# Performance work log

Measured on AMD Instinct MI355X. Metric: run time of the kernel, lower is better.

## Reference

```python
import jax, jax.numpy as jnp
import numpy as np

P = 16          # patch_size
IMG = 224       # image_size
NP = IMG // P   # 14 patches per side
TOTAL = NP * NP # 196
D = P * P * 3   # 768 features per patch


def setup_inputs() -> dict:
    key = jax.random.key(0)
    k1, k2, k3 = jax.random.split(key, 3)
    B = 256
    x = jax.random.normal(k1, (B, 3, IMG, IMG), dtype=jnp.float32)
    # Stacked per-patch Linear(768, 1) weights/biases (196 unshared extractors).
    weight = jax.random.normal(k2, (TOTAL, D), dtype=jnp.float32) * (1.0 / np.sqrt(D))
    bias = jax.random.normal(k3, (TOTAL,), dtype=jnp.float32) * 0.01
    return {"x": x, "weight": weight, "bias": bias}


def _extract_patches(x):
    # Faithful replication of torch: unfold(2,P,P).unfold(3,P,P) ->
    # [B,C,nH,nW,P,P]; permute(0,4,5,1,2,3) -> [B,P,P,C,nH,nW];
    # contiguous().view(B, 196, C, P, P)  (note: this view scrambles axes,
    # as in the original module; we replicate the exact reinterpretation).
    B, C, H, W = x.shape
    nH, nW = H // P, W // P
    p = x.reshape(B, C, nH, P, nW, P).transpose(0, 1, 2, 4, 3, 5)  # [B,C,nH,nW,P,P]
    p = p.transpose(0, 4, 5, 1, 2, 3)                               # [B,P,P,C,nH,nW]
    return p.reshape(B, TOTAL, D)                                   # flatten per 'patch'


def reference(x, weight, bias):
    patches = _extract_patches(x)                   # [B, 196, 768]
    # 196 unshared Linear(768,1) projections as one batched dot-product.
    scores = jnp.einsum('bpd,pd->bp', patches, weight) + bias  # [B, 196]
    return scores
```

## Files before the change

kernel.cpp:

```cpp
#include <hip/hip_runtime.h>


#define NPATCH 196
#define NF4IMG 37632
#define BSTR   197

__global__ __launch_bounds__(256) void prep_kernel(
    const float* __restrict__ weight,
    float* __restrict__ wlay)
{
    const int f = blockIdx.x * 256 + threadIdx.x;
    const int j    = f & 15;
    const int i    = (f >> 4) & 15;
    const int rest = f >> 8;
    const int w  = rest % 14;
    const int ch = rest / 14;
    const int h  = ch % 14;
    const int c  = ch / 14;
    wlay[f] = weight[i * 9408 + j * 588 + c * 196 + h * 14 + w];
}

__global__ __launch_bounds__(896) void run_kernel(
    const float* __restrict__ x,
    const float* __restrict__ wlay,
    const float* __restrict__ bias,
    float* __restrict__ out)
{
    __shared__ float bins[14 * BSTR];
    const int tid  = threadIdx.x;
    const int b    = blockIdx.x;
    const int wv   = tid >> 6;
    const int lane = tid & 63;
    const int i    = lane >> 2;
    const int j4   = lane & 3;

    for (int k = tid; k < 14 * BSTR; k += 896) bins[k] = 0.0f;
    __syncthreads();

    const int h = wv;
    float* mybins = bins + wv * BSTR;

    for (int c = 0; c < 3; ++c) {
        const int tile = c * 14 + h;
        const float4* __restrict__ x4 = (const float4*)x + (size_t)b * NF4IMG
                                        + c * 12544 + (16 * h + i) * 56 + j4;
        const float4* __restrict__ w4 = (const float4*)wlay + tile * 896 + i * 4 + j4;

        int p0[4], ws_[4];
        #pragma unroll
        for (int dj = 0; dj < 4; ++dj) {
            const int jj = 4 * j4 + dj;
            const int t0 = i * 9408 + jj * 588 + c * 196 + h * 14;
            p0[dj]  = t0 / 768;
            ws_[dj] = 768 * (p0[dj] + 1) - t0;
        }

        float accA[4] = {0.f, 0.f, 0.f, 0.f};
        float accB[4] = {0.f, 0.f, 0.f, 0.f};
        #pragma unroll
        for (int w = 0; w < 14; ++w) {
            const float4 xv  = x4[4 * w];
            const float4 wv_ = w4[64 * w];
            const float xs[4]  = {xv.x, xv.y, xv.z, xv.w};
            const float wsv[4] = {wv_.x, wv_.y, wv_.z, wv_.w};
            #pragma unroll
            for (int dj = 0; dj < 4; ++dj) {
                const float v   = xs[dj] * wsv[dj];
                const float sel = (w < ws_[dj]) ? 1.0f : 0.0f;
                accA[dj] = fmaf(v, sel, accA[dj]);
                accB[dj] = fmaf(v, 1.0f - sel, accB[dj]);
            }
        }

        #pragma unroll
        for (int dj = 0; dj < 4; ++dj) {
            unsafeAtomicAdd(&mybins[p0[dj]], accA[dj]);
            if (ws_[dj] < 14)
                unsafeAtomicAdd(&mybins[p0[dj] + 1], accB[dj]);
        }
    }
    __syncthreads();

    for (int p = tid; p < NPATCH; p += 896) {
        float s = 0.0f;
        #pragma unroll
        for (int k = 0; k < 14; ++k) s += bins[k * BSTR + p];
        out[b * NPATCH + p] = s + bias[p];
    }
}

extern "C" void kernel_launch(void* const* d_in, const int* in_sizes, int n_in,
                              void* d_out, int out_size, void* d_ws, size_t ws_size,
                              hipStream_t stream) {
    const float* x      = (const float*)d_in[0];
    const float* weight = (const float*)d_in[1];
    const float* bias   = (const float*)d_in[2];
    float* out          = (float*)d_out;
    float* wlay         = (float*)d_ws;

    prep_kernel<<<588, 256, 0, stream>>>(weight, wlay);
    run_kernel<<<256, 896, 0, stream>>>(x, wlay, bias, out);
}
```

Before: 37.78 us.

## Split each image across two blocks with atomic output, bias init in prep kernel

The main kernel now launches two 448-thread blocks per image, each covering half of the 14 patch rows. The halves combine their partial sums with global atomic adds into the output. The prep kernel pre-fills the output with bias and rewrites the weight permutation as coalesced float4 reads with scattered writes. The aim is more, smaller blocks for better occupancy and latency hiding, at the cost of global atomics and a dependence on the prep kernel initializing the output.

```diff
diff --git a/kernel.cpp b/kernel.cpp
--- a/kernel.cpp
+++ b/kernel.cpp
@@ -7,39 +7,61 @@
 
 __global__ __launch_bounds__(256) void prep_kernel(
     const float* __restrict__ weight,
-    float* __restrict__ wlay)
+    const float* __restrict__ bias,
+    float* __restrict__ wlay,
+    float* __restrict__ out)
 {
-    const int f = blockIdx.x * 256 + threadIdx.x;
-    const int j    = f & 15;
-    const int i    = (f >> 4) & 15;
-    const int rest = f >> 8;
-    const int w  = rest % 14;
-    const int ch = rest / 14;
-    const int h  = ch % 14;
-    const int c  = ch / 14;
-    wlay[f] = weight[i * 9408 + j * 588 + c * 196 + h * 14 + w];
+    const int bid = blockIdx.x;
+    if (bid < 147) {
+        const int t4 = bid * 256 + threadIdx.x;
+        const float4 wv = ((const float4*)weight)[t4];
+        const float wt[4] = {wv.x, wv.y, wv.z, wv.w};
+        #pragma unroll
+        for (int u = 0; u < 4; ++u) {
+            const int t    = 4 * t4 + u;
+            const int i    = t / 9408;
+            const int rem  = t - i * 9408;
+            const int jj   = rem / 588;
+            const int rem2 = rem - jj * 588;
+            const int c    = rem2 / 196;
+            const int rem3 = rem2 - c * 196;
+            const int h    = rem3 / 14;
+            const int w    = rem3 - h * 14;
+            wlay[((c * 14 + h) * 14 + w) * 256 + i * 16 + jj] = wt[u];
+        }
+    } else {
+        const int g4 = (bid - 147) * 256 + threadIdx.x;
+        const int g  = 4 * g4;
+        float4 o;
+        o.x = bias[(g + 0) % NPATCH];
+        o.y = bias[(g + 1) % NPATCH];
+        o.z = bias[(g + 2) % NPATCH];
+        o.w = bias[(g + 3) % NPATCH];
+        ((float4*)out)[g4] = o;
+    }
 }
 
-__global__ __launch_bounds__(896) void run_kernel(
+__global__ __launch_bounds__(448) void run_kernel(
     const float* __restrict__ x,
     const float* __restrict__ wlay,
-    const float* __restrict__ bias,
     float* __restrict__ out)
 {
-    __shared__ float bins[14 * BSTR];
+    __shared__ float bins[7 * BSTR];
     const int tid  = threadIdx.x;
-    const int b    = blockIdx.x;
+    const int b    = blockIdx.x >> 1;
+    const int hh   = blockIdx.x & 1;
     const int wv   = tid >> 6;
     const int lane = tid & 63;
     const int i    = lane >> 2;
     const int j4   = lane & 3;
+    const int h    = hh * 7 + wv;
 
-    for (int k = tid; k < 14 * BSTR; k += 896) bins[k] = 0.0f;
+    for (int k = tid; k < 7 * BSTR; k += 448) bins[k] = 0.0f;
     __syncthreads();
 
-    const int h = wv;
     float* mybins = bins + wv * BSTR;
 
+    #pragma unroll
     for (int c = 0; c < 3; ++c) {
         const int tile = c * 14 + h;
         const float4* __restrict__ x4 = (const float4*)x + (size_t)b * NF4IMG
@@ -81,11 +103,11 @@
     }
     __syncthreads();
 
-    for (int p = tid; p < NPATCH; p += 896) {
+    for (int p = tid; p < NPATCH; p += 448) {
         float s = 0.0f;
         #pragma unroll
-        for (int k = 0; k < 14; ++k) s += bins[k * BSTR + p];
-        out[b * NPATCH + p] = s + bias[p];
+        for (int k = 0; k < 7; ++k) s += bins[k * BSTR + p];
+        unsafeAtomicAdd(&out[b * NPATCH + p], s);
     }
 }
 
@@ -98,6 +120,6 @@
     float* out          = (float*)d_out;
     float* wlay         = (float*)d_ws;
 
-    prep_kernel<<<588, 256, 0, stream>>>(weight, wlay);
-    run_kernel<<<256, 896, 0, stream>>>(x, wlay, bias, out);
+    prep_kernel<<<196, 256, 0, stream>>>(weight, bias, wlay, out);
+    run_kernel<<<512, 448, 0, stream>>>(x, wlay, out);
 }
```

Result: faster. 35.93 us (median of 2 runs) (-4.9%).
